# Performance work log

Measured on AMD Instinct MI355X. Metric: run time of the kernel, lower is better.

The kernel has to match this reference:

```python
import jax, jax.numpy as jnp
import numpy as np

B, S, D = 2, 2048, 2048
NH, HD = 32, 64          # query heads, head_dim
NKV, NREP = 8, 4         # kv heads, num_key_value_groups
ROPE_THETA = 10000.0


def _rope_cos_sin(seq_len, head_dim, dtype=jnp.float32):
    inv_freq = 1.0 / (ROPE_THETA ** (jnp.arange(0, head_dim, 2, dtype=jnp.float32) / head_dim))
    pos = jnp.arange(seq_len, dtype=jnp.float32)
    freqs = jnp.outer(pos, inv_freq)               # [S, HD/2]
    emb = jnp.concatenate([freqs, freqs], axis=-1)  # [S, HD]
    return jnp.cos(emb).astype(dtype), jnp.sin(emb).astype(dtype)


def _rotate_half(x):
    x1, x2 = jnp.split(x, 2, axis=-1)
    return jnp.concatenate([-x2, x1], axis=-1)


def setup_inputs() -> dict:
    key = jax.random.key(0)
    k1, k2, k3, k4, k5 = jax.random.split(key, 5)
    scale = 0.02
    hidden_states = jax.random.normal(k1, (B, S, D), dtype=jnp.float32)
    Wq = jax.random.normal(k2, (NH * HD, D), dtype=jnp.float32) * scale
    Wk = jax.random.normal(k3, (NKV * HD, D), dtype=jnp.float32) * scale
    Wv = jax.random.normal(k4, (NKV * HD, D), dtype=jnp.float32) * scale
    Wo = jax.random.normal(k5, (D, NH * HD), dtype=jnp.float32) * scale
    # additive causal mask [B, 1, S, S]: 0 on/below diagonal, large negative above
    causal = jnp.triu(jnp.full((S, S), -1e9, dtype=jnp.float32), k=1)
    attention_mask = jnp.broadcast_to(causal[None, None], (B, 1, S, S))
    return {"hidden_states": hidden_states, "Wq": Wq, "Wk": Wk, "Wv": Wv,
            "Wo": Wo, "attention_mask": attention_mask}


def reference(hidden_states, Wq, Wk, Wv, Wo, attention_mask):
    bsz, q_len, _ = hidden_states.shape
    # projections (torch Linear: x @ W^T)
    q = (hidden_states @ Wq.T).reshape(bsz, q_len, NH, HD).transpose(0, 2, 1, 3)   # [B,NH,S,HD]
    k = (hidden_states @ Wk.T).reshape(bsz, q_len, NKV, HD).transpose(0, 2, 1, 3)  # [B,NKV,S,HD]
    v = (hidden_states @ Wv.T).reshape(bsz, q_len, NKV, HD).transpose(0, 2, 1, 3)
    # RoPE
    cos, sin = _rope_cos_sin(q_len, HD, hidden_states.dtype)  # [S,HD]
    cos = cos[None, None]  # [1,1,S,HD] (unsqueeze_dim=1 over broadcast batch)
    sin = sin[None, None]
    q = q * cos + _rotate_half(q) * sin
    k = k * cos + _rotate_half(k) * sin
    # repeat_kv (GQA): [B,NKV,S,HD] -> [B,NH,S,HD]
    k = jnp.repeat(k, NREP, axis=1)
    v = jnp.repeat(v, NREP, axis=1)
    # eager attention with materialized scores (faithful to the source)
    scores = jnp.einsum('bhqd,bhkd->bhqk', q, k) / jnp.sqrt(jnp.float32(HD))
    scores = scores + attention_mask[:, :, :, :q_len]
    probs = jax.nn.softmax(scores.astype(jnp.float32), axis=-1).astype(q.dtype)
    out = jnp.einsum('bhqk,bhkd->bhqd', probs, v)          # [B,NH,S,HD]
    out = out.transpose(0, 2, 1, 3).reshape(bsz, q_len, NH * HD)
    return out @ Wo.T
```

## Files before the change

### kernel.cpp

```cpp
#include <hip/hip_runtime.h>


#define S_LEN 2048
#define D_MODEL 2048
#define NHEAD 32
#define HEAD_DIM 64
#define NKVH 8
#define M_ROWS 4096
#define KVW (NKVH * HEAD_DIM)

typedef __attribute__((ext_vector_type(4))) float f32x4;
typedef __attribute__((ext_vector_type(8))) short bf16x8;

#define MFMA16(a, b, c) __builtin_amdgcn_mfma_f32_16x16x32_bf16((a), (b), (c), 0, 0, 0)

#define GLOAD_LDS16(g, l)                                                     \
    __builtin_amdgcn_global_load_lds(                                         \
        (const __attribute__((address_space(1))) void*)(g),                   \
        (__attribute__((address_space(3))) void*)(l), 16, 0, 0)

static __device__ __forceinline__ unsigned short f2bf(float f) {
    union { __bf16 b; unsigned short u; } v;
    v.b = (__bf16)f;
    return v.u;
}

static __device__ __forceinline__ float fexp2(float x) {
#if __has_builtin(__builtin_amdgcn_exp2f)
    return __builtin_amdgcn_exp2f(x);
#else
    return exp2f(x);
#endif
}

static __device__ bool detect_f32_block(const unsigned short* __restrict__ h) {
    __shared__ int dcnt;
    if (threadIdx.x == 0) dcnt = 0;
    __syncthreads();
    const unsigned short v = h[2 * (threadIdx.x & 255)];
    const int e = (v >> 7) & 0xFF;
    if (threadIdx.x < 256 && e >= 0x8D) atomicAdd(&dcnt, 1);
    __syncthreads();
    return dcnt >= 8;
}

static __device__ __forceinline__ bf16x8 load_frag(bool f32p, const void* p, size_t off) {
    if (f32p) {
        const float* fp = (const float*)p + off;
        f32x4 x = *reinterpret_cast<const f32x4*>(fp);
        f32x4 y = *reinterpret_cast<const f32x4*>(fp + 4);
        bf16x8 r;
        r[0] = (short)f2bf(x[0]); r[1] = (short)f2bf(x[1]);
        r[2] = (short)f2bf(x[2]); r[3] = (short)f2bf(x[3]);
        r[4] = (short)f2bf(y[0]); r[5] = (short)f2bf(y[1]);
        r[6] = (short)f2bf(y[2]); r[7] = (short)f2bf(y[3]);
        return r;
    }
    return *reinterpret_cast<const bf16x8*>((const unsigned short*)p + off);
}

__global__ __launch_bounds__(256) void rope_init(float2* __restrict__ tab) {
    const int i = blockIdx.x * 256 + threadIdx.x;
    const int s = i >> 5, dd = i & 31;
    const float inv = exp2f(-(float)dd * 0.4152410118609203f);
    const float th = (float)s * inv;
    float sn, cs;
    sincosf(th, &sn, &cs);
    tab[i] = make_float2(cs, sn);
}

__global__ __launch_bounds__(256) void cvt_all(const void* __restrict__ h,
                                               const void* __restrict__ wq,
                                               const void* __restrict__ wk,
                                               const void* __restrict__ wv,
                                               const void* __restrict__ wo,
                                               unsigned short* __restrict__ hbuf,
                                               unsigned short* __restrict__ wqb,
                                               unsigned short* __restrict__ wkvb,
                                               unsigned short* __restrict__ wob) {
    const bool f32p = detect_f32_block((const unsigned short*)h);
    const int e0 = 1048576;
    const int e1 = e0 + 524288;
    const int e2 = e1 + 131072;
    const int e3 = e2 + 131072;
    const int e4 = e3 + 524288;
    int i = blockIdx.x * 256 + threadIdx.x;
    const int stride = gridDim.x * 256;
    for (; i < e4; i += stride) {
        const void* s;
        unsigned short* d;
        size_t off;
        if (i < e0)      { s = h;  d = hbuf; off = (size_t)i; }
        else if (i < e1) { s = wq; d = wqb;  off = (size_t)(i - e0); }
        else if (i < e2) { s = wk; d = wkvb; off = (size_t)(i - e1); }
        else if (i < e3) { s = wv; d = wkvb + (size_t)512 * 2048; off = (size_t)(i - e2); }
        else             { s = wo; d = wob;  off = (size_t)(i - e3); }
        bf16x8 v = load_frag(f32p, s, off * 8);
        *reinterpret_cast<bf16x8*>(d + off * 8) = v;
    }
}

static __device__ __forceinline__ void rope4_tab(const float2* __restrict__ tab,
                                                 const float (&vals)[4], float (&outv)[4],
                                                 int m, int l16) {
    const int s = m & (S_LEN - 1);
#pragma unroll
    for (int nt = 0; nt < 4; ++nt) {
        const int d = nt * 16 + l16;
        const float2 cs = tab[s * 32 + (d & 31)];
        const float part = vals[nt ^ 2];
        const float rot = (nt < 2) ? -part : part;
        outv[nt] = vals[nt] * cs.x + rot * cs.y;
    }
}

static __device__ __forceinline__ void rope4(const float (&vals)[4], float (&outv)[4],
                                             int m, int l16) {
    const float sf = (float)(m & (S_LEN - 1));
#pragma unroll
    for (int nt = 0; nt < 4; ++nt) {
        const int d = nt * 16 + l16;
        const float inv = exp2f(-(float)(d & 31) * 0.4152410118609203f);
        const float th = sf * inv;
        float sn, cs;
        sincosf(th, &sn, &cs);
        const float part = vals[nt ^ 2];
        const float rot = (nt < 2) ? -part : part;
        outv[nt] = vals[nt] * cs + rot * sn;
    }
}

__global__ __launch_bounds__(256) void gemm_qkv_lds(const unsigned short* __restrict__ A,
                                                    const unsigned short* __restrict__ W,
                                                    unsigned short* __restrict__ Qo,
                                                    unsigned short* __restrict__ KVo,
                                                    const float2* __restrict__ ropetab) {
    __shared__ unsigned short lds_a[128 * 32];
    __shared__ unsigned short lds_b[128 * 32];

    const int wave = threadIdx.x >> 6;
    const int lane = threadIdx.x & 63;
    const int l16  = lane & 15;
    const int quad = lane >> 4;
    const int wm   = wave >> 1;
    const int wn   = wave & 1;

    const int m0 = blockIdx.x * 128;
    const int n0 = blockIdx.y * 128;

    const int srow = lane >> 2;
    const int scol = (lane & 3) * 8;
    const unsigned short* ag[2];
    const unsigned short* wg[2];
#pragma unroll
    for (int i = 0; i < 2; ++i) {
        const int c = wave * 2 + i;
        ag[i] = A + (size_t)(m0 + c * 16 + srow) * D_MODEL + scol;
        wg[i] = W + (size_t)(n0 + c * 16 + srow) * D_MODEL + scol;
    }

    f32x4 acc[4][4];
#pragma unroll
    for (int i = 0; i < 4; ++i)
#pragma unroll
        for (int j = 0; j < 4; ++j) acc[i][j] = (f32x4){0.f, 0.f, 0.f, 0.f};

    for (int k0 = 0; k0 < D_MODEL; k0 += 32) {
#pragma unroll
        for (int i = 0; i < 2; ++i) {
            const int c = wave * 2 + i;
            GLOAD_LDS16(ag[i] + k0, &lds_a[c * 512]);
            GLOAD_LDS16(wg[i] + k0, &lds_b[c * 512]);
        }
        __syncthreads();

        bf16x8 af[4], bfm[4];
#pragma unroll
        for (int t = 0; t < 4; ++t) {
            af[t]  = *reinterpret_cast<const bf16x8*>(&lds_a[(wm * 64 + t * 16 + l16) * 32 + quad * 8]);
            bfm[t] = *reinterpret_cast<const bf16x8*>(&lds_b[(wn * 64 + t * 16 + l16) * 32 + quad * 8]);
        }
#pragma unroll
        for (int mt = 0; mt < 4; ++mt)
#pragma unroll
            for (int nt = 0; nt < 4; ++nt)
                acc[mt][nt] = MFMA16(af[mt], bfm[nt], acc[mt][nt]);
        __syncthreads();
    }

    const int ncol0 = n0 + wn * 64;
    const bool do_rope = (ncol0 < 2048 + KVW);
    unsigned short* dst;
    int cstride, c0;
    if (ncol0 < 2048) { dst = Qo;  cstride = 2048; c0 = ncol0; }
    else              { dst = KVo; cstride = 1024; c0 = ncol0 - 2048; }

#pragma unroll
    for (int mt = 0; mt < 4; ++mt) {
#pragma unroll
        for (int r = 0; r < 4; ++r) {
            const int m = m0 + wm * 64 + mt * 16 + quad * 4 + r;
            float vals[4];
#pragma unroll
            for (int nt = 0; nt < 4; ++nt) vals[nt] = acc[mt][nt][r];
            float outv[4];
            if (do_rope) {
                rope4_tab(ropetab, vals, outv, m, l16);
            } else {
#pragma unroll
                for (int nt = 0; nt < 4; ++nt) outv[nt] = vals[nt];
            }
            unsigned short* cp = dst + (size_t)m * cstride + c0;
#pragma unroll
            for (int nt = 0; nt < 4; ++nt) cp[nt * 16 + l16] = f2bf(outv[nt]);
        }
    }
}

__global__ __launch_bounds__(256) void gemm_bt_lds(const unsigned short* __restrict__ A,
                                                   const unsigned short* __restrict__ W,
                                                   void* __restrict__ Cp, int N,
                                                   const unsigned short* __restrict__ hdet,
                                                   int rope, int finalout) {
    __shared__ unsigned short lds_a[128 * 32];
    __shared__ unsigned short lds_b[128 * 32];

    bool of32 = false;
    if (finalout) of32 = detect_f32_block(hdet);

    const int wave = threadIdx.x >> 6;
    const int lane = threadIdx.x & 63;
    const int l16  = lane & 15;
    const int quad = lane >> 4;
    const int wm   = wave >> 1;
    const int wn   = wave & 1;

    const int m0 = blockIdx.x * 128;
    const int n0 = blockIdx.y * 128;

    const int srow = lane >> 2;
    const int scol = (lane & 3) * 8;
    const unsigned short* ag[2];
    const unsigned short* wg[2];
#pragma unroll
    for (int i = 0; i < 2; ++i) {
        const int c = wave * 2 + i;
        ag[i] = A + (size_t)(m0 + c * 16 + srow) * D_MODEL + scol;
        wg[i] = W + (size_t)(n0 + c * 16 + srow) * D_MODEL + scol;
    }

    f32x4 acc[4][4];
#pragma unroll
    for (int i = 0; i < 4; ++i)
#pragma unroll
        for (int j = 0; j < 4; ++j) acc[i][j] = (f32x4){0.f, 0.f, 0.f, 0.f};

    for (int k0 = 0; k0 < D_MODEL; k0 += 32) {
#pragma unroll
        for (int i = 0; i < 2; ++i) {
            const int c = wave * 2 + i;
            GLOAD_LDS16(ag[i] + k0, &lds_a[c * 512]);
            GLOAD_LDS16(wg[i] + k0, &lds_b[c * 512]);
        }
        __syncthreads();

        bf16x8 af[4], bfm[4];
#pragma unroll
        for (int t = 0; t < 4; ++t) {
            af[t]  = *reinterpret_cast<const bf16x8*>(&lds_a[(wm * 64 + t * 16 + l16) * 32 + quad * 8]);
            bfm[t] = *reinterpret_cast<const bf16x8*>(&lds_b[(wn * 64 + t * 16 + l16) * 32 + quad * 8]);
        }
#pragma unroll
        for (int mt = 0; mt < 4; ++mt)
#pragma unroll
            for (int nt = 0; nt < 4; ++nt)
                acc[mt][nt] = MFMA16(af[mt], bfm[nt], acc[mt][nt]);
        __syncthreads();
    }

    const bool do_rope = (rope != 0);
    const int ncol0 = n0 + wn * 64;

#pragma unroll
    for (int mt = 0; mt < 4; ++mt) {
#pragma unroll
        for (int r = 0; r < 4; ++r) {
            const int m = m0 + wm * 64 + mt * 16 + quad * 4 + r;
            float vals[4];
#pragma unroll
            for (int nt = 0; nt < 4; ++nt) vals[nt] = acc[mt][nt][r];
            float outv[4];
            if (do_rope) {
                rope4(vals, outv, m, l16);
            } else {
#pragma unroll
                for (int nt = 0; nt < 4; ++nt) outv[nt] = vals[nt];
            }
            const size_t crow = (size_t)m * N + ncol0;
            if (of32) {
                float* cp = (float*)Cp + crow;
#pragma unroll
                for (int nt = 0; nt < 4; ++nt) cp[nt * 16 + l16] = outv[nt];
            } else {
                unsigned short* cp = (unsigned short*)Cp + crow;
#pragma unroll
                for (int nt = 0; nt < 4; ++nt) cp[nt * 16 + l16] = f2bf(outv[nt]);
            }
        }
    }
}

__global__ __launch_bounds__(256) void transpose_v(const unsigned short* __restrict__ Vsrc,
                                                   unsigned short* __restrict__ Vt) {
    __shared__ unsigned short t[64][72];
    const int bid = blockIdx.x;
    const int ct = bid & 7;
    const int st = (bid >> 3) & 31;
    const int b  = bid >> 8;
    const unsigned short* src = Vsrc + ((size_t)b * S_LEN + st * 64) * 1024 + ct * 64;
    unsigned short* dst = Vt + ((size_t)b * KVW + ct * 64) * S_LEN + st * 64;
    const int r0 = threadIdx.x >> 3;
    const int c0 = (threadIdx.x & 7) * 8;
#pragma unroll
    for (int h = 0; h < 2; ++h) {
        bf16x8 v = *reinterpret_cast<const bf16x8*>(src + (size_t)(r0 + h * 32) * 1024 + c0);
        *reinterpret_cast<bf16x8*>(&t[r0 + h * 32][c0]) = v;
    }
    __syncthreads();
#pragma unroll
    for (int h = 0; h < 2; ++h) {
        const int cr = r0 + h * 32;
        bf16x8 v;
#pragma unroll
        for (int j = 0; j < 8; ++j) v[j] = (short)t[c0 + j][cr];
        *reinterpret_cast<bf16x8*>(dst + (size_t)cr * S_LEN + c0) = v;
    }
}

struct AttnCtx {
    const unsigned short* qbase;
    const unsigned short* kbase;
    const unsigned short* vtbase;
    unsigned short* obase;
    int kvs;
    int l16, quad;
    unsigned short (*lpw)[72];
};

#define SM_C 0.18033688011112042f
#define SM_THR 8.0f

static __device__ __forceinline__ void attn_qtile(const AttnCtx& cx, int q0w) {
    const int l16 = cx.l16, quad = cx.quad;
    const int kvs = cx.kvs;

    bf16x8 ones;
#pragma unroll
    for (int j = 0; j < 8; ++j) ones[j] = (short)0x3F80;

    bf16x8 aq[2][2];
#pragma unroll
    for (int m = 0; m < 2; ++m)
#pragma unroll
        for (int kh = 0; kh < 2; ++kh)
            aq[m][kh] = *reinterpret_cast<const bf16x8*>(
                cx.qbase + (size_t)(q0w + m * 16 + l16) * D_MODEL + kh * 32 + quad * 8);

    f32x4 o[2][4];
    f32x4 c_l[2];
#pragma unroll
    for (int m = 0; m < 2; ++m) {
#pragma unroll
        for (int i = 0; i < 4; ++i) o[m][i] = (f32x4){0.f, 0.f, 0.f, 0.f};
        c_l[m] = (f32x4){0.f, 0.f, 0.f, 0.f};
    }
    float m2[2][4];
#pragma unroll
    for (int m = 0; m < 2; ++m)
#pragma unroll
        for (int r = 0; r < 4; ++r) m2[m][r] = 0.f;

    const int kv_hi = q0w + 32;

    bf16x8 kfa[8], kfb[8];

#define LOADK(DST, KK0)                                                       \
    {                                                                         \
        _Pragma("unroll")                                                     \
        for (int t = 0; t < 4; ++t) {                                         \
            const unsigned short* krow =                                      \
                cx.kbase + (size_t)((KK0) + t * 16 + l16) * kvs;              \
            DST[2 * t]     = *reinterpret_cast<const bf16x8*>(krow + quad * 8);       \
            DST[2 * t + 1] = *reinterpret_cast<const bf16x8*>(krow + 32 + quad * 8);  \
        }                                                                     \
    }

#define ATTN_BODY(CUR, NXT)                                                   \
    {                                                                         \
        f32x4 sc[2][4];                                                       \
        __builtin_amdgcn_s_setprio(1);                                        \
        _Pragma("unroll")                                                     \
        for (int t = 0; t < 4; ++t) {                                         \
            _Pragma("unroll")                                                 \
            for (int m = 0; m < 2; ++m) {                                     \
                f32x4 c = (f32x4){0.f, 0.f, 0.f, 0.f};                        \
                c = MFMA16(aq[m][0], CUR[2 * t], c);                          \
                c = MFMA16(aq[m][1], CUR[2 * t + 1], c);                      \
                sc[m][t] = c;                                                 \
            }                                                                 \
        }                                                                     \
        __builtin_amdgcn_s_setprio(0);                                        \
        if (k0 + 64 < kv_hi) LOADK(NXT, k0 + 64);                             \
        bf16x8 vf[8];                                                         \
        _Pragma("unroll")                                                     \
        for (int nt = 0; nt < 4; ++nt) {                                      \
            const unsigned short* vrow =                                      \
                cx.vtbase + (size_t)(nt * 16 + l16) * S_LEN + k0 + quad * 8;  \
            vf[2 * nt]     = *reinterpret_cast<const bf16x8*>(vrow);          \
            vf[2 * nt + 1] = *reinterpret_cast<const bf16x8*>(vrow + 32);     \
        }                                                                     \
        const bool full = (k0 + 63 <= q0w);                                   \
        float pm[2][4];                                                       \
        float dif = -3.0e38f;                                                 \
        _Pragma("unroll")                                                     \
        for (int m = 0; m < 2; ++m) {                                         \
            _Pragma("unroll")                                                 \
            for (int r = 0; r < 4; ++r) {                                     \
                const int qi = q0w + m * 16 + quad * 4 + r;                   \
                float s[4];                                                   \
                _Pragma("unroll")                                             \
                for (int t = 0; t < 4; ++t) {                                 \
                    s[t] = sc[m][t][r] * SM_C;                                \
                    if (!full && (k0 + t * 16 + l16 > qi)) s[t] = -1.0e30f;   \
                    sc[m][t][r] = s[t];                                       \
                }                                                             \
                const float p = fmaxf(fmaxf(s[0], s[1]), fmaxf(s[2], s[3])); \
                pm[m][r] = p;                                                 \
                dif = fmaxf(dif, p - m2[m][r]);                               \
            }                                                                 \
        }                                                                     \
        if (__any(dif > SM_THR)) {                                            \
            _Pragma("unroll")                                                 \
            for (int m = 0; m < 2; ++m) {                                     \
                _Pragma("unroll")                                             \
                for (int r = 0; r < 4; ++r) {                                 \
                    float mt = pm[m][r];                                      \
                    _Pragma("unroll")                                         \
                    for (int off = 1; off < 16; off <<= 1)                    \
                        mt = fmaxf(mt, __shfl_xor(mt, off, 64));              \
                    const float mn = fmaxf(m2[m][r], mt);                     \
                    const float al = fexp2(m2[m][r] - mn);                    \
                    m2[m][r] = mn;                                            \
                    _Pragma("unroll")                                         \
                    for (int nt = 0; nt < 4; ++nt) o[m][nt][r] *= al;         \
                    c_l[m][r] *= al;                                          \
                }                                                             \
            }                                                                 \
        }                                                                     \
                                    \
        _Pragma("unroll")                                                     \
        for (int m = 0; m < 2; ++m) {                                         \
            _Pragma("unroll")                                                 \
            for (int r = 0; r < 4; ++r) {                                     \
                const float mb = m2[m][r];                                    \
                _Pragma("unroll")                                             \
                for (int t = 0; t < 4; ++t) {                                 \
                    const float pv = fexp2(sc[m][t][r] - mb);                 \
                    cx.lpw[m * 16 + quad * 4 + r][t * 16 + l16] = f2bf(pv);   \
                }                                                             \
            }                                                                 \
        }                                                                     \
        asm volatile("" ::: "memory");                                        \
        bf16x8 ap[2][2];                                                      \
        _Pragma("unroll")                                                     \
        for (int m = 0; m < 2; ++m)                                           \
            _Pragma("unroll")                                                 \
            for (int kh = 0; kh < 2; ++kh)                                    \
                ap[m][kh] = *reinterpret_cast<const bf16x8*>(                 \
                    &cx.lpw[m * 16 + l16][kh * 32 + quad * 8]);               \
        __builtin_amdgcn_s_setprio(1);                                        \
        _Pragma("unroll")                                                     \
        for (int nt = 0; nt < 4; ++nt)                                        \
            _Pragma("unroll")                                                 \
            for (int m = 0; m < 2; ++m) {                                     \
                o[m][nt] = MFMA16(ap[m][0], vf[2 * nt], o[m][nt]);            \
                o[m][nt] = MFMA16(ap[m][1], vf[2 * nt + 1], o[m][nt]);        \
            }                                                                 \
        _Pragma("unroll")                                                     \
        for (int m = 0; m < 2; ++m) {                                         \
            c_l[m] = MFMA16(ap[m][0], ones, c_l[m]);                          \
            c_l[m] = MFMA16(ap[m][1], ones, c_l[m]);                          \
        }                                                                     \
        __builtin_amdgcn_s_setprio(0);                                        \
    }

    LOADK(kfa, 0);
    int k0 = 0;
    for (;;) {
        ATTN_BODY(kfa, kfb);
        k0 += 64;
        if (k0 >= kv_hi) break;
        ATTN_BODY(kfb, kfa);
        k0 += 64;
        if (k0 >= kv_hi) break;
    }
#undef ATTN_BODY
#undef LOADK

#pragma unroll
    for (int m = 0; m < 2; ++m)
#pragma unroll
        for (int r = 0; r < 4; ++r) {
            const float inv_l = 1.0f / c_l[m][r];
            unsigned short* orow = cx.obase + (size_t)(q0w + m * 16 + quad * 4 + r) * D_MODEL;
#pragma unroll
            for (int nt = 0; nt < 4; ++nt)
                orow[nt * 16 + l16] = f2bf(o[m][nt][r] * inv_l);
        }
}

__global__ __launch_bounds__(256) void attn_kernel4(const unsigned short* __restrict__ Q,
                                                    const unsigned short* __restrict__ Kb,
                                                    const unsigned short* __restrict__ Vt,
                                                    unsigned short* __restrict__ O, int kvs) {
    __shared__ unsigned short lp[4][32][72];

    const int wave = threadIdx.x >> 6;
    const int lane = threadIdx.x & 63;

    const int bid = blockIdx.x;
    const int p   = bid & 7;
    const int h   = (bid >> 3) & (NHEAD - 1);
    const int b   = bid >> 8;
    const int kvh = h >> 2;

    AttnCtx cx;
    cx.qbase  = Q + (size_t)b * S_LEN * D_MODEL + h * HEAD_DIM;
    cx.kbase  = Kb + (size_t)b * S_LEN * kvs + kvh * HEAD_DIM;
    cx.vtbase = Vt + ((size_t)b * KVW + kvh * HEAD_DIM) * S_LEN;
    cx.obase  = O + (size_t)b * S_LEN * D_MODEL + h * HEAD_DIM;
    cx.kvs    = kvs;
    cx.l16    = lane & 15;
    cx.quad   = lane >> 4;
    cx.lpw    = lp[wave];

    attn_qtile(cx, p * 128 + wave * 32);
    attn_qtile(cx, (15 - p) * 128 + wave * 32);
}

__global__ __launch_bounds__(256) void gemm_bt(const void* __restrict__ Ap,
                                               const void* __restrict__ Wp,
                                               void* __restrict__ Cp, int N,
                                               const unsigned short* __restrict__ hdet,
                                               int a_input, int rope, int finalout) {
    const bool isf32 = detect_f32_block(hdet);
    const bool af32 = isf32 && (a_input != 0);
    const bool wf32 = isf32;
    const bool of32 = isf32 && (finalout != 0);

    const int wave = threadIdx.x >> 6;
    const int lane = threadIdx.x & 63;
    const int l16  = lane & 15;
    const int quad = lane >> 4;
    const int m0 = blockIdx.x * 64 + wave * 16;
    const int n0 = blockIdx.y * 64;

    f32x4 acc[4];
#pragma unroll
    for (int i = 0; i < 4; ++i) acc[i] = (f32x4){0.f, 0.f, 0.f, 0.f};

    const size_t aoff = (size_t)(m0 + l16) * D_MODEL + quad * 8;
    size_t woff[4];
#pragma unroll
    for (int nt = 0; nt < 4; ++nt)
        woff[nt] = (size_t)(n0 + nt * 16 + l16) * D_MODEL + quad * 8;

    for (int k0 = 0; k0 < D_MODEL; k0 += 32) {
        bf16x8 a = load_frag(af32, Ap, aoff + k0);
#pragma unroll
        for (int nt = 0; nt < 4; ++nt) {
            bf16x8 b = load_frag(wf32, Wp, woff[nt] + k0);
            acc[nt] = MFMA16(a, b, acc[nt]);
        }
    }

#pragma unroll
    for (int r = 0; r < 4; ++r) {
        const int m = m0 + quad * 4 + r;
        float vals[4];
#pragma unroll
        for (int nt = 0; nt < 4; ++nt) vals[nt] = acc[nt][r];
        float outv[4];
        if (rope) {
            rope4(vals, outv, m, l16);
        } else {
#pragma unroll
            for (int nt = 0; nt < 4; ++nt) outv[nt] = vals[nt];
        }
        const size_t crow = (size_t)m * N + n0;
        if (of32) {
            float* cp = (float*)Cp + crow;
#pragma unroll
            for (int nt = 0; nt < 4; ++nt) cp[nt * 16 + l16] = outv[nt];
        } else {
            unsigned short* cp = (unsigned short*)Cp + crow;
#pragma unroll
            for (int nt = 0; nt < 4; ++nt) cp[nt * 16 + l16] = f2bf(outv[nt]);
        }
    }
}

__global__ __launch_bounds__(256) void attn_kernel(const unsigned short* __restrict__ Q,
                                                   const unsigned short* __restrict__ Kb,
                                                   const unsigned short* __restrict__ Vb,
                                                   unsigned short* __restrict__ O, int kvs) {
    __shared__ unsigned short lp[4][16][32];

    const int wave = threadIdx.x >> 6;
    const int lane = threadIdx.x & 63;
    const int l16  = lane & 15;
    const int quad = lane >> 4;

    const int bid = blockIdx.x;
    const int qb  = bid & 31;
    const int h   = (bid >> 5) & 31;
    const int b   = bid >> 10;
    const int kvh = h >> 2;
    const int q0  = qb * 64 + wave * 16;

    const unsigned short* qbase = Q + (size_t)b * S_LEN * D_MODEL + h * HEAD_DIM;
    const unsigned short* kbase = Kb + (size_t)b * S_LEN * kvs + kvh * HEAD_DIM;
    const unsigned short* vbase = Vb + (size_t)b * S_LEN * kvs + kvh * HEAD_DIM;

    bf16x8 aq0 = *reinterpret_cast<const bf16x8*>(qbase + (size_t)(q0 + l16) * D_MODEL + quad * 8);
    bf16x8 aq1 = *reinterpret_cast<const bf16x8*>(qbase + (size_t)(q0 + l16) * D_MODEL + 32 + quad * 8);

    f32x4 o[4];
#pragma unroll
    for (int i = 0; i < 4; ++i) o[i] = (f32x4){0.f, 0.f, 0.f, 0.f};
    float mrow[4], lrow[4];
#pragma unroll
    for (int r = 0; r < 4; ++r) { mrow[r] = -3.0e38f; lrow[r] = 0.f; }

    const int kv_hi = qb * 64 + 64;
    for (int k0 = 0; k0 < kv_hi; k0 += 32) {
        f32x4 sc[2];
#pragma unroll
        for (int t = 0; t < 2; ++t) {
            const unsigned short* krow = kbase + (size_t)(k0 + t * 16 + l16) * kvs;
            bf16x8 b0 = *reinterpret_cast<const bf16x8*>(krow + quad * 8);
            bf16x8 b1 = *reinterpret_cast<const bf16x8*>(krow + 32 + quad * 8);
            f32x4 c = (f32x4){0.f, 0.f, 0.f, 0.f};
            c = MFMA16(aq0, b0, c);
            c = MFMA16(aq1, b1, c);
            sc[t] = c;
        }

        float alpha[4], p0v[4], p1v[4];
#pragma unroll
        for (int r = 0; r < 4; ++r) {
            const int qi = q0 + quad * 4 + r;
            float s0 = sc[0][r] * 0.125f;
            float s1 = sc[1][r] * 0.125f;
            if (k0 + l16 > qi)       s0 = -1.0e30f;
            if (k0 + 16 + l16 > qi)  s1 = -1.0e30f;
            float mt = fmaxf(s0, s1);
#pragma unroll
            for (int off = 1; off < 16; off <<= 1) mt = fmaxf(mt, __shfl_xor(mt, off, 64));
            const float mn = fmaxf(mrow[r], mt);
            const float al = __expf(mrow[r] - mn);
            const float p0 = __expf(s0 - mn);
            const float p1 = __expf(s1 - mn);
            float rs = p0 + p1;
#pragma unroll
            for (int off = 1; off < 16; off <<= 1) rs += __shfl_xor(rs, off, 64);
            lrow[r] = lrow[r] * al + rs;
            mrow[r] = mn;
            alpha[r] = al;
            p0v[r] = p0; p1v[r] = p1;
        }
#pragma unroll
        for (int nt = 0; nt < 4; ++nt)
#pragma unroll
            for (int r = 0; r < 4; ++r) o[nt][r] *= alpha[r];

        __syncthreads();
#pragma unroll
        for (int r = 0; r < 4; ++r) {
            lp[wave][quad * 4 + r][l16]      = f2bf(p0v[r]);
            lp[wave][quad * 4 + r][16 + l16] = f2bf(p1v[r]);
        }
        __syncthreads();
        bf16x8 ap = *reinterpret_cast<const bf16x8*>(&lp[wave][l16][quad * 8]);

#pragma unroll
        for (int nt = 0; nt < 4; ++nt) {
            const unsigned short* vcol = vbase + nt * 16 + l16 + (size_t)(k0 + quad * 8) * kvs;
            bf16x8 bv;
#pragma unroll
            for (int j = 0; j < 8; ++j) bv[j] = (short)vcol[(size_t)j * kvs];
            o[nt] = MFMA16(ap, bv, o[nt]);
        }
    }

    unsigned short* obase = O + (size_t)b * S_LEN * D_MODEL + h * HEAD_DIM;
#pragma unroll
    for (int r = 0; r < 4; ++r) {
        const float inv_l = 1.0f / lrow[r];
        unsigned short* orow = obase + (size_t)(q0 + quad * 4 + r) * D_MODEL;
#pragma unroll
        for (int nt = 0; nt < 4; ++nt)
            orow[nt * 16 + l16] = f2bf(o[nt][r] * inv_l);
    }
}

extern "C" void kernel_launch(void* const* d_in, const int* in_sizes, int n_in,
                              void* d_out, int out_size, void* d_ws, size_t ws_size,
                              hipStream_t stream) {
    const void* hidden = d_in[0];
    const void* Wq = d_in[1];
    const void* Wk = d_in[2];
    const void* Wv = d_in[3];
    const void* Wo = d_in[4];

    char* ws = (char*)d_ws;
    dim3 blk(256);

    const size_t NEED = 1024 + ((size_t)64 << 20) + (512u << 10);
    if (ws_size >= NEED) {
        unsigned short* kvbuf = (unsigned short*)(ws + 1024);
        unsigned short* abuf  = kvbuf + (size_t)4096 * 1024;
        unsigned short* hbuf  = abuf + (size_t)4096 * 2048;
        unsigned short* wqb   = hbuf + (size_t)4096 * 2048;
        unsigned short* wkvb  = wqb + (size_t)2048 * 2048;
        unsigned short* wob   = wkvb + (size_t)1024 * 2048;
        unsigned short* vtbuf = wob + (size_t)2048 * 2048;
        float2* ropetab       = (float2*)(vtbuf + (size_t)2 * 512 * 2048);
        unsigned short* qbuf  = (unsigned short*)d_out;

        rope_init<<<dim3(256), blk, 0, stream>>>(ropetab);
        cvt_all<<<dim3(2048), blk, 0, stream>>>(hidden, Wq, Wk, Wv, Wo,
                                                hbuf, wqb, wkvb, wob);

        gemm_qkv_lds<<<dim3(32, 24), blk, 0, stream>>>(hbuf, wqb, qbuf, kvbuf, ropetab);
        transpose_v<<<dim3(512), blk, 0, stream>>>(kvbuf + 512, vtbuf);
        attn_kernel4<<<dim3(2 * NHEAD * (S_LEN / 256)), blk, 0, stream>>>(qbuf, kvbuf, vtbuf, abuf, 1024);
        gemm_bt_lds<<<dim3(32, 16), blk, 0, stream>>>(abuf, wob, d_out, 2048,
                                                      (const unsigned short*)hidden, 0, 1);
    } else {
        unsigned short* kbuf = (unsigned short*)(ws + 1024);
        unsigned short* vbuf = (unsigned short*)(ws + 1024 + (4u << 20));
        unsigned short* abuf = (unsigned short*)(ws + 1024 + (8u << 20));
        unsigned short* qbuf = (unsigned short*)d_out;
        const unsigned short* hdet = (const unsigned short*)hidden;
        gemm_bt<<<dim3(M_ROWS / 64, D_MODEL / 64), blk, 0, stream>>>(hidden, Wq, qbuf, D_MODEL, hdet, 1, 1, 0);
        gemm_bt<<<dim3(M_ROWS / 64, (NKVH * HEAD_DIM) / 64), blk, 0, stream>>>(hidden, Wk, kbuf, NKVH * HEAD_DIM, hdet, 1, 1, 0);
        gemm_bt<<<dim3(M_ROWS / 64, (NKVH * HEAD_DIM) / 64), blk, 0, stream>>>(hidden, Wv, vbuf, NKVH * HEAD_DIM, hdet, 1, 0, 0);
        attn_kernel<<<dim3(2 * NHEAD * (S_LEN / 64)), blk, 0, stream>>>(qbuf, kbuf, vbuf, abuf, 512);
        gemm_bt<<<dim3(M_ROWS / 64, D_MODEL / 64), blk, 0, stream>>>(abuf, Wo, d_out, D_MODEL, hdet, 0, 0, 1);
    }
}
```

Before: 421.0 us.

## Fuse rope table into conversion, XCD-swizzle GEMM tiles, split attention per q-tile

Moves RoPE cos/sin table generation into the conversion kernel, removing one launch. Adds an XCD-aware block remap to both LDS GEMMs so neighbouring tiles land on the same chiplet and share L2. Changes the attention launch from paired q-tiles (p and 15-p) per block to one q-tile per block, with the heaviest tiles scheduled first and a launch bound of 3 blocks per SM. The single-tile attention relies on longest-first ordering for load balance and doubles the block count. The swizzle assumes the block count divides by 8.

```diff
diff --git a/kernel.cpp b/kernel.cpp
--- a/kernel.cpp
+++ b/kernel.cpp
@@ -31,6 +31,15 @@
 #else
     return exp2f(x);
 #endif
+}
+
+static __device__ __forceinline__ void xcd_swz(int& bx, int& by) {
+    const int gx = gridDim.x;
+    const int nwg = gx * gridDim.y;
+    int lin = blockIdx.y * gx + blockIdx.x;
+    lin = (lin & 7) * (nwg >> 3) + (lin >> 3);
+    bx = lin % gx;
+    by = lin / gx;
 }
 
 static __device__ bool detect_f32_block(const unsigned short* __restrict__ h) {
@@ -59,16 +68,6 @@
     return *reinterpret_cast<const bf16x8*>((const unsigned short*)p + off);
 }
 
-__global__ __launch_bounds__(256) void rope_init(float2* __restrict__ tab) {
-    const int i = blockIdx.x * 256 + threadIdx.x;
-    const int s = i >> 5, dd = i & 31;
-    const float inv = exp2f(-(float)dd * 0.4152410118609203f);
-    const float th = (float)s * inv;
-    float sn, cs;
-    sincosf(th, &sn, &cs);
-    tab[i] = make_float2(cs, sn);
-}
-
 __global__ __launch_bounds__(256) void cvt_all(const void* __restrict__ h,
                                                const void* __restrict__ wq,
                                                const void* __restrict__ wk,
@@ -77,16 +76,32 @@
                                                unsigned short* __restrict__ hbuf,
                                                unsigned short* __restrict__ wqb,
                                                unsigned short* __restrict__ wkvb,
-                                               unsigned short* __restrict__ wob) {
+                                               unsigned short* __restrict__ wob,
+                                               float2* __restrict__ ropetab) {
     const bool f32p = detect_f32_block((const unsigned short*)h);
     const int e0 = 1048576;
     const int e1 = e0 + 524288;
     const int e2 = e1 + 131072;
     const int e3 = e2 + 131072;
     const int e4 = e3 + 524288;
+    const int e5 = e4 + 8192;
     int i = blockIdx.x * 256 + threadIdx.x;
     const int stride = gridDim.x * 256;
-    for (; i < e4; i += stride) {
+    for (; i < e5; i += stride) {
+        if (i >= e4) {
+            const int base = (i - e4) * 8;
+#pragma unroll
+            for (int j = 0; j < 8; ++j) {
+                const int idx = base + j;
+                const int s = idx >> 5, dd = idx & 31;
+                const float inv = exp2f(-(float)dd * 0.4152410118609203f);
+                const float th = (float)s * inv;
+                float sn, cs;
+                sincosf(th, &sn, &cs);
+                ropetab[idx] = make_float2(cs, sn);
+            }
+            continue;
+        }
         const void* s;
         unsigned short* d;
         size_t off;
@@ -145,8 +160,10 @@
     const int wm   = wave >> 1;
     const int wn   = wave & 1;
 
-    const int m0 = blockIdx.x * 128;
-    const int n0 = blockIdx.y * 128;
+    int bx, by;
+    xcd_swz(bx, by);
+    const int m0 = bx * 128;
+    const int n0 = by * 128;
 
     const int srow = lane >> 2;
     const int scol = (lane & 3) * 8;
@@ -235,8 +252,10 @@
     const int wm   = wave >> 1;
     const int wn   = wave & 1;
 
-    const int m0 = blockIdx.x * 128;
-    const int n0 = blockIdx.y * 128;
+    int bx, by;
+    xcd_swz(bx, by);
+    const int m0 = bx * 128;
+    const int n0 = by * 128;
 
     const int srow = lane >> 2;
     const int scol = (lane & 3) * 8;
@@ -519,19 +538,19 @@
         }
 }
 
-__global__ __launch_bounds__(256) void attn_kernel4(const unsigned short* __restrict__ Q,
-                                                    const unsigned short* __restrict__ Kb,
-                                                    const unsigned short* __restrict__ Vt,
-                                                    unsigned short* __restrict__ O, int kvs) {
+__global__ __launch_bounds__(256, 3) void attn_kernel6(const unsigned short* __restrict__ Q,
+                                                       const unsigned short* __restrict__ Kb,
+                                                       const unsigned short* __restrict__ Vt,
+                                                       unsigned short* __restrict__ O, int kvs) {
     __shared__ unsigned short lp[4][32][72];
 
     const int wave = threadIdx.x >> 6;
     const int lane = threadIdx.x & 63;
 
     const int bid = blockIdx.x;
-    const int p   = bid & 7;
-    const int h   = (bid >> 3) & (NHEAD - 1);
-    const int b   = bid >> 8;
+    const int qt  = 15 - (bid & 15);
+    const int h   = (bid >> 4) & (NHEAD - 1);
+    const int b   = bid >> 9;
     const int kvh = h >> 2;
 
     AttnCtx cx;
@@ -544,8 +563,7 @@
     cx.quad   = lane >> 4;
     cx.lpw    = lp[wave];
 
-    attn_qtile(cx, p * 128 + wave * 32);
-    attn_qtile(cx, (15 - p) * 128 + wave * 32);
+    attn_qtile(cx, qt * 128 + wave * 32);
 }
 
 __global__ __launch_bounds__(256) void gemm_bt(const void* __restrict__ Ap,
@@ -738,13 +756,12 @@
         float2* ropetab       = (float2*)(vtbuf + (size_t)2 * 512 * 2048);
         unsigned short* qbuf  = (unsigned short*)d_out;
 
-        rope_init<<<dim3(256), blk, 0, stream>>>(ropetab);
         cvt_all<<<dim3(2048), blk, 0, stream>>>(hidden, Wq, Wk, Wv, Wo,
-                                                hbuf, wqb, wkvb, wob);
+                                                hbuf, wqb, wkvb, wob, ropetab);
 
         gemm_qkv_lds<<<dim3(32, 24), blk, 0, stream>>>(hbuf, wqb, qbuf, kvbuf, ropetab);
         transpose_v<<<dim3(512), blk, 0, stream>>>(kvbuf + 512, vtbuf);
-        attn_kernel4<<<dim3(2 * NHEAD * (S_LEN / 256)), blk, 0, stream>>>(qbuf, kvbuf, vtbuf, abuf, 1024);
+        attn_kernel6<<<dim3(2 * NHEAD * (S_LEN / 128)), blk, 0, stream>>>(qbuf, kvbuf, vtbuf, abuf, 1024);
         gemm_bt_lds<<<dim3(32, 16), blk, 0, stream>>>(abuf, wob, d_out, 2048,
                                                       (const unsigned short*)hidden, 0, 1);
     } else {
```

After: 1.119 ms. 166% more time.
